# Kernel optimization log

Measured on AMD Instinct MI355X. Metric: run time of the kernel, lower is better.

The kernel has to match this reference:

```python
import jax, jax.numpy as jnp
import numpy as np

N_NODES = 50000
N_EDGES = 800000
IN_DIM = 256
HID = 64
NEG_SLOPE = 0.2


def setup_inputs() -> dict:
    key = jax.random.key(0)
    ks = jax.random.split(key, 16)
    s = lambda d: 1.0 / np.sqrt(d)
    x = jax.random.normal(ks[0], (N_NODES, IN_DIM), dtype=jnp.float32)
    src = jax.random.randint(ks[1], (N_EDGES,), 0, N_NODES, dtype=jnp.int32)
    dst = jax.random.randint(ks[2], (N_EDGES,), 0, N_NODES, dtype=jnp.int32)
    # layer 0: in 256 -> 4 heads x 64, no residual, ELU
    W0 = jax.random.normal(ks[3], (IN_DIM, 4 * HID), dtype=jnp.float32) * s(IN_DIM)
    al0 = jax.random.normal(ks[4], (4, HID), dtype=jnp.float32) * s(HID)
    ar0 = jax.random.normal(ks[5], (4, HID), dtype=jnp.float32) * s(HID)
    b0 = jnp.zeros((4 * HID,), dtype=jnp.float32)
    # layer 1: in 256 -> 4 heads x 64, identity residual (256 == 4*64), ELU
    W1 = jax.random.normal(ks[6], (4 * HID, 4 * HID), dtype=jnp.float32) * s(4 * HID)
    al1 = jax.random.normal(ks[7], (4, HID), dtype=jnp.float32) * s(HID)
    ar1 = jax.random.normal(ks[8], (4, HID), dtype=jnp.float32) * s(HID)
    b1 = jnp.zeros((4 * HID,), dtype=jnp.float32)
    # layer 2 (output): in 256 -> 1 head x 64, linear residual, no activation
    W2 = jax.random.normal(ks[9], (4 * HID, HID), dtype=jnp.float32) * s(4 * HID)
    al2 = jax.random.normal(ks[10], (1, HID), dtype=jnp.float32) * s(HID)
    ar2 = jax.random.normal(ks[11], (1, HID), dtype=jnp.float32) * s(HID)
    b2 = jnp.zeros((HID,), dtype=jnp.float32)
    res_w2 = jax.random.normal(ks[12], (4 * HID, HID), dtype=jnp.float32) * s(4 * HID)
    return {"x": x, "src": src, "dst": dst,
            "W0": W0, "al0": al0, "ar0": ar0, "b0": b0,
            "W1": W1, "al1": al1, "ar1": ar1, "b1": b1,
            "W2": W2, "al2": al2, "ar2": ar2, "b2": b2,
            "res_w2": res_w2}


def gat_layer(h, src, dst, W, al, ar, bias, residual, res_w, activation):
    H, D = al.shape
    feat = (h @ W).reshape(-1, H, D)               # [N,H,D]
    el = jnp.sum(feat * al[None], axis=-1)         # [N,H]
    er = jnp.sum(feat * ar[None], axis=-1)         # [N,H]
    e = jax.nn.leaky_relu(el[src] + er[dst], NEG_SLOPE)  # [E,H]
    # segment softmax over incoming edges of each destination node
    emax = jax.ops.segment_max(e, dst, num_segments=N_NODES)  # [N,H]
    ee = jnp.exp(e - emax[dst])
    denom = jax.ops.segment_sum(ee, dst, num_segments=N_NODES)
    alpha = ee / denom[dst]                        # [E,H]
    msg = feat[src] * alpha[..., None]             # [E,H,D]
    out = jax.ops.segment_sum(msg, dst, num_segments=N_NODES)  # [N,H,D]
    if residual:
        if res_w is not None:
            out = out + (h @ res_w).reshape(-1, 1, D)
        else:
            out = out + h.reshape(-1, H, D)
    out = out + bias.reshape(H, D)
    if activation:
        out = jax.nn.elu(out)
    return out.reshape(-1, H * D)                  # flatten(1)


def reference(x, src, dst, W0, al0, ar0, b0, W1, al1, ar1, b1,
              W2, al2, ar2, b2, res_w2):
    h = gat_layer(x, src, dst, W0, al0, ar0, b0, False, None, True)
    h = gat_layer(h, src, dst, W1, al1, ar1, b1, True, None, True)
    h = gat_layer(h, src, dst, W2, al2, ar2, b2, True, res_w2, False)
    return h  # [N, 64]
```

## Files before the change

kernel.cpp:

```cpp
#include <hip/hip_runtime.h>
#include <math.h>

#define NNODES 50000
#define NEDGES 800000

__device__ __forceinline__ float leaky(float x) { return x > 0.f ? x : 0.2f * x; }

__device__ __forceinline__ ushort f2bf(float f) {
    unsigned u = __float_as_uint(f);
    return (ushort)((u + 0x7fffu + ((u >> 16) & 1u)) >> 16);
}
__device__ __forceinline__ float bf2f(ushort u) {
    return __uint_as_float((unsigned)u << 16);
}

__global__ void hist_kernel(const int* __restrict__ dst, int* __restrict__ counts) {
    int e = blockIdx.x * 256 + threadIdx.x;
    if (e < NEDGES) atomicAdd(&counts[dst[e]], 1);
}

__global__ __launch_bounds__(256) void scan_partial(const int* __restrict__ counts,
                                                    int* __restrict__ bsum, int Nn) {
    int b = blockIdx.x, t = threadIdx.x;
    int base = b * 1024;
    int v = 0;
#pragma unroll
    for (int i = 0; i < 4; ++i) {
        int idx = base + t + 256 * i;
        if (idx < Nn) v += counts[idx];
    }
    for (int o = 32; o; o >>= 1) v += __shfl_xor(v, o);
    __shared__ int ws[4];
    if ((t & 63) == 0) ws[t >> 6] = v;
    __syncthreads();
    if (t == 0) bsum[b] = ws[0] + ws[1] + ws[2] + ws[3];
}

__global__ __launch_bounds__(256) void scan_final(const int* __restrict__ counts,
                                                  const int* __restrict__ bsum,
                                                  int* __restrict__ row_start, int Nn, int nB) {
    __shared__ int off_s;
    __shared__ int tsum[256];
    int b = blockIdx.x, t = threadIdx.x;
    if (t == 0) {
        int o = 0;
        for (int i = 0; i < b; ++i) o += bsum[i];
        off_s = o;
    }
    int base = b * 1024 + t * 4;
    int c0 = 0, c1 = 0, c2 = 0, c3 = 0;
    if (base + 3 < Nn) {
        int4 c = *reinterpret_cast<const int4*>(counts + base);
        c0 = c.x; c1 = c.y; c2 = c.z; c3 = c.w;
    } else {
        if (base + 0 < Nn) c0 = counts[base + 0];
        if (base + 1 < Nn) c1 = counts[base + 1];
        if (base + 2 < Nn) c2 = counts[base + 2];
        if (base + 3 < Nn) c3 = counts[base + 3];
    }
    int s0 = c0, s1 = s0 + c1, s2 = s1 + c2, s3 = s2 + c3;
    tsum[t] = s3;
    __syncthreads();
    for (int o = 1; o < 256; o <<= 1) {
        int u = (t >= o) ? tsum[t - o] : 0;
        __syncthreads();
        tsum[t] += u;
        __syncthreads();
    }
    int o = off_s + tsum[t] - s3;
    if (base + 3 < Nn) {
        *reinterpret_cast<int4*>(row_start + base) = make_int4(o, o + s0, o + s1, o + s2);
    } else {
        if (base + 0 < Nn) row_start[base + 0] = o;
        if (base + 1 < Nn) row_start[base + 1] = o + s0;
        if (base + 2 < Nn) row_start[base + 2] = o + s1;
        if (base + 3 < Nn) row_start[base + 3] = o + s2;
    }
    if (b == nB - 1 && t == 255) row_start[Nn] = off_s + tsum[255];
}

__global__ void scatter_kernel(const int* __restrict__ src, const int* __restrict__ dst,
                               const int* __restrict__ row_start, int* __restrict__ cursor,
                               int* __restrict__ csr_src) {
    int e = blockIdx.x * 256 + threadIdx.x;
    if (e < NEDGES) {
        int d = dst[e];
        int pos = row_start[d] + atomicAdd(&cursor[d], 1);
        csr_src[pos] = src[e];
    }
}

__global__ void pack_kernel(const float* __restrict__ W0, const float* __restrict__ W1,
                            const float* __restrict__ W2, const float* __restrict__ Wr,
                            ushort* __restrict__ Bt0, ushort* __restrict__ Bt1,
                            ushort* __restrict__ Bt2) {
    int idx = blockIdx.x * 256 + threadIdx.x;
    if (idx < 65536) {
        int n = idx >> 8, k = idx & 255;
        Bt0[idx] = f2bf(W0[k * 256 + n]);
    } else if (idx < 131072) {
        int j = idx - 65536;
        int n = j >> 8, k = j & 255;
        Bt1[j] = f2bf(W1[k * 256 + n]);
    } else {
        int j = idx - 131072;
        int n = j >> 8, k = j & 255;
        Bt2[j] = f2bf(n < 64 ? W2[k * 64 + n] : Wr[k * 64 + (n - 64)]);
    }
}

template <int MCOLS>
__global__ __launch_bounds__(256) void gemm_mfma(const float* __restrict__ A,
                                                 const ushort* __restrict__ Bt,
                                                 const float* __restrict__ al,
                                                 const float* __restrict__ ar,
                                                 ushort* __restrict__ featb,
                                                 float* __restrict__ el, float* __restrict__ er,
                                                 float* __restrict__ resid, int Nrows) {
    using bf16x8 = __attribute__((ext_vector_type(8))) short;
    using f32x4 = __attribute__((ext_vector_type(4))) float;
    __shared__ ushort As[8192];
    __shared__ ushort Bs[8192];
    const int tid = threadIdx.x;
    const int lane = tid & 63;
    const int wave = tid >> 6;
    const int wr = wave >> 1, wc = wave & 1;
    const int q = lane >> 4, li = lane & 15;
    const int r0 = blockIdx.x * 128;
    const int n0 = blockIdx.y * 128;

    f32x4 acc[4][4];
#pragma unroll
    for (int i = 0; i < 4; ++i)
#pragma unroll
        for (int j = 0; j < 4; ++j) acc[i][j] = (f32x4){0.f, 0.f, 0.f, 0.f};

    for (int kk = 0; kk < 256; kk += 64) {
        __syncthreads();
#pragma unroll
        for (int j = 0; j < 4; ++j) {
            int g = j * 256 + tid;
            int m = g >> 3, kg = g & 7;
            int mf = m >> 4, mr = m & 15;
            int row = r0 + m;
            float4 v0 = make_float4(0.f, 0.f, 0.f, 0.f), v1 = v0;
            if (row < Nrows) {
                const float* p = A + (size_t)row * 256 + kk + kg * 8;
                v0 = *reinterpret_cast<const float4*>(p);
                v1 = *reinterpret_cast<const float4*>(p + 4);
            }
            union { bf16x8 v; ushort u[8]; } pk;
            pk.u[0] = f2bf(v0.x); pk.u[1] = f2bf(v0.y);
            pk.u[2] = f2bf(v0.z); pk.u[3] = f2bf(v0.w);
            pk.u[4] = f2bf(v1.x); pk.u[5] = f2bf(v1.y);
            pk.u[6] = f2bf(v1.z); pk.u[7] = f2bf(v1.w);
            *reinterpret_cast<bf16x8*>(&As[((mf * 8 + kg) * 16 + (mr ^ kg)) * 8]) = pk.v;
        }
#pragma unroll
        for (int j = 0; j < 4; ++j) {
            int g = j * 256 + tid;
            int n = g >> 3, kg = g & 7;
            int nf = n >> 4, nr = n & 15;
            bf16x8 v = *reinterpret_cast<const bf16x8*>(Bt + (size_t)(n0 + n) * 256 + kk + kg * 8);
            *reinterpret_cast<bf16x8*>(&Bs[((nf * 8 + kg) * 16 + (nr ^ kg)) * 8]) = v;
        }
        __syncthreads();
#pragma unroll
        for (int t = 0; t < 2; ++t) {
            const int kc = t * 4 + q;
            bf16x8 af[4], bfv[4];
#pragma unroll
            for (int f = 0; f < 4; ++f) {
                af[f] = *reinterpret_cast<const bf16x8*>(
                    &As[(((wr * 4 + f) * 8 + kc) * 16 + (li ^ kc)) * 8]);
                bfv[f] = *reinterpret_cast<const bf16x8*>(
                    &Bs[(((wc * 4 + f) * 8 + kc) * 16 + (li ^ kc)) * 8]);
            }
#pragma unroll
            for (int f = 0; f < 4; ++f)
#pragma unroll
                for (int f2 = 0; f2 < 4; ++f2)
                    acc[f][f2] =
                        __builtin_amdgcn_mfma_f32_16x16x32_bf16(af[f], bfv[f2], acc[f][f2], 0, 0, 0);
        }
    }

    if constexpr (MCOLS == 256) {
        const int hblk = (n0 >> 6) + wc;
        float alv[4], arv[4];
#pragma unroll
        for (int f2 = 0; f2 < 4; ++f2) {
            alv[f2] = al[hblk * 64 + f2 * 16 + li];
            arv[f2] = ar[hblk * 64 + f2 * 16 + li];
        }
#pragma unroll
        for (int f = 0; f < 4; ++f) {
#pragma unroll
            for (int r = 0; r < 4; ++r) {
                int row = r0 + wr * 64 + f * 16 + q * 4 + r;
                bool ok = row < Nrows;
                float elp = 0.f, erp = 0.f;
#pragma unroll
                for (int f2 = 0; f2 < 4; ++f2) {
                    float v = acc[f][f2][r];
                    elp = fmaf(v, alv[f2], elp);
                    erp = fmaf(v, arv[f2], erp);
                    if (ok) featb[(size_t)row * 256 + (f2 * 16 + li) * 4 + hblk] = f2bf(v);
                }
#pragma unroll
                for (int o = 1; o < 16; o <<= 1) {
                    elp += __shfl_xor(elp, o);
                    erp += __shfl_xor(erp, o);
                }
                if (ok && li == 0) {
                    el[row * 4 + hblk] = elp;
                    er[row * 4 + hblk] = erp;
                }
            }
        }
    } else {
        if (wc == 0) {
            float alv[4], arv[4];
#pragma unroll
            for (int f2 = 0; f2 < 4; ++f2) {
                alv[f2] = al[f2 * 16 + li];
                arv[f2] = ar[f2 * 16 + li];
            }
#pragma unroll
            for (int f = 0; f < 4; ++f) {
#pragma unroll
                for (int r = 0; r < 4; ++r) {
                    int row = r0 + wr * 64 + f * 16 + q * 4 + r;
                    bool ok = row < Nrows;
                    float elp = 0.f, erp = 0.f;
#pragma unroll
                    for (int f2 = 0; f2 < 4; ++f2) {
                        float v = acc[f][f2][r];
                        elp = fmaf(v, alv[f2], elp);
                        erp = fmaf(v, arv[f2], erp);
                        if (ok) featb[(size_t)row * 64 + f2 * 16 + li] = f2bf(v);
                    }
#pragma unroll
                    for (int o = 1; o < 16; o <<= 1) {
                        elp += __shfl_xor(elp, o);
                        erp += __shfl_xor(erp, o);
                    }
                    if (ok && li == 0) {
                        el[row] = elp;
                        er[row] = erp;
                    }
                }
            }
        } else {
#pragma unroll
            for (int f = 0; f < 4; ++f) {
#pragma unroll
                for (int r = 0; r < 4; ++r) {
                    int row = r0 + wr * 64 + f * 16 + q * 4 + r;
                    if (row < Nrows) {
#pragma unroll
                        for (int f2 = 0; f2 < 4; ++f2)
                            resid[(size_t)row * 64 + f2 * 16 + li] = acc[f][f2][r];
                    }
                }
            }
        }
    }
}

template <int RES, bool ACT>
__global__ __launch_bounds__(256) void agg4_kernel(
    const ushort* __restrict__ featb, const float* __restrict__ el,
    const float* __restrict__ er, const int* __restrict__ row_start,
    const int* __restrict__ csr_src, const float* __restrict__ resbuf,
    const float* __restrict__ bias, float* __restrict__ out, int Nn) {
    using ushort8v = __attribute__((ext_vector_type(8))) unsigned short;
    __shared__ float wbuf[4][256];
    __shared__ int obuf[4][64];
    const int wv = threadIdx.x >> 6, lane = threadIdx.x & 63;
    const int g = lane >> 5, li = lane & 31;
    int node = blockIdx.x * 4 + wv;
    if (node >= Nn) return;

    int begin = row_start[node], end = row_start[node + 1];
    float4 ern = *(reinterpret_cast<const float4*>(er) + node);

    float denom[4] = {0.f, 0.f, 0.f, 0.f};
    float acc[2][4] = {{0.f, 0.f, 0.f, 0.f}, {0.f, 0.f, 0.f, 0.f}};

    for (int c = begin; c < end; c += 64) {
        int nE = min(64, end - c);
        float4 w = make_float4(0.f, 0.f, 0.f, 0.f);
        int s = 0;
        if (lane < nE) {
            s = csr_src[c + lane];
            float4 e4 = *(reinterpret_cast<const float4*>(el) + s);
            w.x = __expf(leaky(e4.x + ern.x));
            w.y = __expf(leaky(e4.y + ern.y));
            w.z = __expf(leaky(e4.z + ern.z));
            w.w = __expf(leaky(e4.w + ern.w));
        }
        denom[0] += w.x; denom[1] += w.y; denom[2] += w.z; denom[3] += w.w;
        obuf[wv][lane] = s * 256;
        *reinterpret_cast<float4*>(&wbuf[wv][lane * 4]) = w;
        __asm__ volatile("s_waitcnt lgkmcnt(0)" ::: "memory");

#pragma unroll 4
        for (int e2 = 0; e2 < nE; e2 += 2) {
            int e = e2 + g;
            float4 we = make_float4(0.f, 0.f, 0.f, 0.f);
            int off = 0;
            if (e < nE) {
                off = obuf[wv][e];
                we = *reinterpret_cast<const float4*>(&wbuf[wv][e * 4]);
            }
            ushort8v v = *reinterpret_cast<const ushort8v*>(featb + off + li * 8);
            acc[0][0] = fmaf(we.x, bf2f(v[0]), acc[0][0]);
            acc[0][1] = fmaf(we.y, bf2f(v[1]), acc[0][1]);
            acc[0][2] = fmaf(we.z, bf2f(v[2]), acc[0][2]);
            acc[0][3] = fmaf(we.w, bf2f(v[3]), acc[0][3]);
            acc[1][0] = fmaf(we.x, bf2f(v[4]), acc[1][0]);
            acc[1][1] = fmaf(we.y, bf2f(v[5]), acc[1][1]);
            acc[1][2] = fmaf(we.z, bf2f(v[6]), acc[1][2]);
            acc[1][3] = fmaf(we.w, bf2f(v[7]), acc[1][3]);
        }
        __asm__ volatile("" ::: "memory");
    }

#pragma unroll
    for (int j = 0; j < 2; ++j)
#pragma unroll
        for (int h = 0; h < 4; ++h) acc[j][h] += __shfl_xor(acc[j][h], 32);
#pragma unroll
    for (int h = 0; h < 4; ++h)
        for (int o = 32; o; o >>= 1) denom[h] += __shfl_xor(denom[h], o);

    bool has = end > begin;
#pragma unroll
    for (int hh = 0; hh < 2; ++hh) {
        int h = g * 2 + hh;
        float d0 = denom[h];
        float o0 = has ? acc[0][h] / d0 : 0.f;
        float o1 = has ? acc[1][h] / d0 : 0.f;
        int dbase = h * 64 + li * 2;
        if constexpr (RES == 1) {
            float2 rv = *reinterpret_cast<const float2*>(resbuf + (size_t)node * 256 + dbase);
            o0 += rv.x; o1 += rv.y;
        }
        float2 bv = *reinterpret_cast<const float2*>(bias + dbase);
        o0 += bv.x; o1 += bv.y;
        if constexpr (ACT) {
            o0 = o0 > 0.f ? o0 : __expf(o0) - 1.f;
            o1 = o1 > 0.f ? o1 : __expf(o1) - 1.f;
        }
        *reinterpret_cast<float2*>(out + (size_t)node * 256 + dbase) = make_float2(o0, o1);
    }
}

__global__ __launch_bounds__(256) void agg1_kernel(
    const ushort* __restrict__ featb, const float* __restrict__ el,
    const float* __restrict__ er, const int* __restrict__ row_start,
    const int* __restrict__ csr_src, const float* __restrict__ resbuf,
    const float* __restrict__ bias, float* __restrict__ out, int Nn) {
    __shared__ float wbuf[4][64];
    __shared__ int obuf[4][64];
    const int wv = threadIdx.x >> 6, lane = threadIdx.x & 63;
    const int g = lane >> 4, li = lane & 15;
    int node = blockIdx.x * 4 + wv;
    if (node >= Nn) return;

    int begin = row_start[node], end = row_start[node + 1];
    float ern = er[node];
    float denom = 0.f;
    float acc[4] = {0.f, 0.f, 0.f, 0.f};

    for (int c = begin; c < end; c += 64) {
        int nE = min(64, end - c);
        float w = 0.f;
        int s = 0;
        if (lane < nE) {
            s = csr_src[c + lane];
            w = __expf(leaky(el[s] + ern));
        }
        denom += w;
        obuf[wv][lane] = s * 64;
        wbuf[wv][lane] = w;
        __asm__ volatile("s_waitcnt lgkmcnt(0)" ::: "memory");

#pragma unroll 2
        for (int e4i = 0; e4i < nE; e4i += 4) {
            int e = e4i + g;
            float we = 0.f;
            int off = 0;
            if (e < nE) {
                off = obuf[wv][e];
                we = wbuf[wv][e];
            }
            ushort4 v = *reinterpret_cast<const ushort4*>(featb + off + li * 4);
            acc[0] = fmaf(we, bf2f(v.x), acc[0]);
            acc[1] = fmaf(we, bf2f(v.y), acc[1]);
            acc[2] = fmaf(we, bf2f(v.z), acc[2]);
            acc[3] = fmaf(we, bf2f(v.w), acc[3]);
        }
        __asm__ volatile("" ::: "memory");
    }

#pragma unroll
    for (int j = 0; j < 4; ++j) {
        acc[j] += __shfl_xor(acc[j], 16);
        acc[j] += __shfl_xor(acc[j], 32);
    }
    for (int o = 32; o; o >>= 1) denom += __shfl_xor(denom, o);

    if (g == 0) {
        bool has = end > begin;
        float4 rv = *reinterpret_cast<const float4*>(resbuf + (size_t)node * 64 + li * 4);
        float4 bv = *reinterpret_cast<const float4*>(bias + li * 4);
        float4 o4;
        o4.x = (has ? acc[0] / denom : 0.f) + rv.x + bv.x;
        o4.y = (has ? acc[1] / denom : 0.f) + rv.y + bv.y;
        o4.z = (has ? acc[2] / denom : 0.f) + rv.z + bv.z;
        o4.w = (has ? acc[3] / denom : 0.f) + rv.w + bv.w;
        *reinterpret_cast<float4*>(out + (size_t)node * 64 + li * 4) = o4;
    }
}

extern "C" void kernel_launch(void* const* d_in, const int* in_sizes, int n_in, void* d_out,
                              int out_size, void* d_ws, size_t ws_size, hipStream_t stream) {
    const float* x   = (const float*)d_in[0];
    const int* src   = (const int*)d_in[1];
    const int* dst   = (const int*)d_in[2];
    const float* W0  = (const float*)d_in[3];
    const float* al0 = (const float*)d_in[4];
    const float* ar0 = (const float*)d_in[5];
    const float* b0  = (const float*)d_in[6];
    const float* W1  = (const float*)d_in[7];
    const float* al1 = (const float*)d_in[8];
    const float* ar1 = (const float*)d_in[9];
    const float* b1  = (const float*)d_in[10];
    const float* W2  = (const float*)d_in[11];
    const float* al2 = (const float*)d_in[12];
    const float* ar2 = (const float*)d_in[13];
    const float* b2  = (const float*)d_in[14];
    const float* Wr2 = (const float*)d_in[15];
    float* out = (float*)d_out;

    char* w = (char*)d_ws;
    size_t off = 0;
    auto alloc = [&](size_t bytes) -> char* {
        char* p = w + off;
        off += (bytes + 255) & ~(size_t)255;
        return p;
    };
    float* hbuf     = (float*)alloc((size_t)NNODES * 256 * 4);
    ushort* featb   = (ushort*)alloc((size_t)NNODES * 256 * 2);
    float* resid    = (float*)alloc((size_t)NNODES * 64 * 4);
    float* el       = (float*)alloc((size_t)NNODES * 4 * 4);
    float* er       = (float*)alloc((size_t)NNODES * 4 * 4);
    ushort* Bt0     = (ushort*)alloc(65536 * 2);
    ushort* Bt1     = (ushort*)alloc(65536 * 2);
    ushort* Bt2     = (ushort*)alloc(32768 * 2);
    int* counts     = (int*)alloc((size_t)NNODES * 4 * 2);
    int* cursor     = counts + NNODES;
    int* row_start  = (int*)alloc((size_t)(NNODES + 1) * 4);
    int* bsum       = (int*)alloc(64 * 4);
    int* csr_src    = (int*)alloc((size_t)NEDGES * 4);

    hipMemsetAsync(counts, 0, (size_t)NNODES * 4 * 2, stream);

    const int EB = (NEDGES + 255) / 256;
    const int NB4 = (NNODES + 3) / 4;
    const int NBM = (NNODES + 127) / 128;
    const int NSB = (NNODES + 1023) / 1024;

    hist_kernel<<<EB, 256, 0, stream>>>(dst, counts);
    scan_partial<<<NSB, 256, 0, stream>>>(counts, bsum, NNODES);
    scan_final<<<NSB, 256, 0, stream>>>(counts, bsum, row_start, NNODES, NSB);
    scatter_kernel<<<EB, 256, 0, stream>>>(src, dst, row_start, cursor, csr_src);
    pack_kernel<<<640, 256, 0, stream>>>(W0, W1, W2, Wr2, Bt0, Bt1, Bt2);

    gemm_mfma<256><<<dim3(NBM, 2), 256, 0, stream>>>(x, Bt0, al0, ar0, featb, el, er,
                                                     nullptr, NNODES);
    agg4_kernel<0, true><<<NB4, 256, 0, stream>>>(featb, el, er, row_start, csr_src,
                                                  nullptr, b0, hbuf, NNODES);
    gemm_mfma<256><<<dim3(NBM, 2), 256, 0, stream>>>(hbuf, Bt1, al1, ar1, featb, el, er,
                                                     nullptr, NNODES);
    agg4_kernel<1, true><<<NB4, 256, 0, stream>>>(featb, el, er, row_start, csr_src,
                                                  hbuf, b1, hbuf, NNODES);
    gemm_mfma<128><<<dim3(NBM, 1), 256, 0, stream>>>(hbuf, Bt2, al2, ar2, featb, el, er,
                                                     resid, NNODES);
    agg1_kernel<<<NB4, 256, 0, stream>>>(featb, el, er, row_start, csr_src,
                                         resid, b2, out, NNODES);
}
```

Baseline: 457.3 us.

## Store hidden activations in bf16 and load GEMM tiles directly into LDS

Hidden-layer activations between layers are now stored as bf16 instead of fp32, halving the buffer traffic for aggregation writes, residual reads and GEMM A-loads. The later GEMMs then stage A and B tiles with global_load_lds straight into shared memory, using an unswizzled layout, which removes the in-register conversion and copy. The scan-partial and weight-pack kernels are merged into one launch. In exchange, the residual path loses precision through bf16 rounding, and the unswizzled LDS layout may cause bank conflicts.

```diff
diff --git a/kernel.cpp b/kernel.cpp
--- a/kernel.cpp
+++ b/kernel.cpp
@@ -3,6 +3,7 @@
 
 #define NNODES 50000
 #define NEDGES 800000
+#define NSB 49
 
 __device__ __forceinline__ float leaky(float x) { return x > 0.f ? x : 0.2f * x; }
 
@@ -14,26 +15,49 @@
     return __uint_as_float((unsigned)u << 16);
 }
 
+typedef const __attribute__((address_space(1))) void* gptr_t;
+typedef __attribute__((address_space(3))) void* lptr_t;
+
 __global__ void hist_kernel(const int* __restrict__ dst, int* __restrict__ counts) {
     int e = blockIdx.x * 256 + threadIdx.x;
     if (e < NEDGES) atomicAdd(&counts[dst[e]], 1);
 }
 
-__global__ __launch_bounds__(256) void scan_partial(const int* __restrict__ counts,
-                                                    int* __restrict__ bsum, int Nn) {
-    int b = blockIdx.x, t = threadIdx.x;
-    int base = b * 1024;
-    int v = 0;
-#pragma unroll
-    for (int i = 0; i < 4; ++i) {
-        int idx = base + t + 256 * i;
-        if (idx < Nn) v += counts[idx];
-    }
-    for (int o = 32; o; o >>= 1) v += __shfl_xor(v, o);
-    __shared__ int ws[4];
-    if ((t & 63) == 0) ws[t >> 6] = v;
-    __syncthreads();
-    if (t == 0) bsum[b] = ws[0] + ws[1] + ws[2] + ws[3];
+__global__ __launch_bounds__(256) void prep_kernel(
+    const int* __restrict__ counts, int* __restrict__ bsum, int Nn,
+    const float* __restrict__ W0, const float* __restrict__ W1, const float* __restrict__ W2,
+    const float* __restrict__ Wr, ushort* __restrict__ Bt0, ushort* __restrict__ Bt1,
+    ushort* __restrict__ Bt2) {
+    int t = threadIdx.x;
+    if (blockIdx.x < NSB) {
+        int b = blockIdx.x;
+        int base = b * 1024;
+        int v = 0;
+#pragma unroll
+        for (int i = 0; i < 4; ++i) {
+            int idx = base + t + 256 * i;
+            if (idx < Nn) v += counts[idx];
+        }
+        for (int o = 32; o; o >>= 1) v += __shfl_xor(v, o);
+        __shared__ int ws[4];
+        if ((t & 63) == 0) ws[t >> 6] = v;
+        __syncthreads();
+        if (t == 0) bsum[b] = ws[0] + ws[1] + ws[2] + ws[3];
+    } else {
+        int idx = (blockIdx.x - NSB) * 256 + t;
+        if (idx < 65536) {
+            int n = idx >> 8, k = idx & 255;
+            Bt0[idx] = f2bf(W0[k * 256 + n]);
+        } else if (idx < 131072) {
+            int j = idx - 65536;
+            int n = j >> 8, k = j & 255;
+            Bt1[j] = f2bf(W1[k * 256 + n]);
+        } else {
+            int j = idx - 131072;
+            int n = j >> 8, k = j & 255;
+            Bt2[j] = f2bf(n < 64 ? W2[k * 64 + n] : Wr[k * 64 + (n - 64)]);
+        }
+    }
 }
 
 __global__ __launch_bounds__(256) void scan_final(const int* __restrict__ counts,
@@ -90,27 +114,8 @@
     }
 }
 
-__global__ void pack_kernel(const float* __restrict__ W0, const float* __restrict__ W1,
-                            const float* __restrict__ W2, const float* __restrict__ Wr,
-                            ushort* __restrict__ Bt0, ushort* __restrict__ Bt1,
-                            ushort* __restrict__ Bt2) {
-    int idx = blockIdx.x * 256 + threadIdx.x;
-    if (idx < 65536) {
-        int n = idx >> 8, k = idx & 255;
-        Bt0[idx] = f2bf(W0[k * 256 + n]);
-    } else if (idx < 131072) {
-        int j = idx - 65536;
-        int n = j >> 8, k = j & 255;
-        Bt1[j] = f2bf(W1[k * 256 + n]);
-    } else {
-        int j = idx - 131072;
-        int n = j >> 8, k = j & 255;
-        Bt2[j] = f2bf(n < 64 ? W2[k * 64 + n] : Wr[k * 64 + (n - 64)]);
-    }
-}
-
-template <int MCOLS>
-__global__ __launch_bounds__(256) void gemm_mfma(const float* __restrict__ A,
+template <int MCOLS, bool ABF16>
+__global__ __launch_bounds__(256) void gemm_mfma(const void* __restrict__ Araw,
                                                  const ushort* __restrict__ Bt,
                                                  const float* __restrict__ al,
                                                  const float* __restrict__ ar,
@@ -121,6 +126,8 @@
     using f32x4 = __attribute__((ext_vector_type(4))) float;
     __shared__ ushort As[8192];
     __shared__ ushort Bs[8192];
+    const float* Af = (const float*)Araw;
+    const ushort* Ab = (const ushort*)Araw;
     const int tid = threadIdx.x;
     const int lane = tid & 63;
     const int wave = tid >> 6;
@@ -137,32 +144,43 @@
 
     for (int kk = 0; kk < 256; kk += 64) {
         __syncthreads();
+        if constexpr (ABF16) {
+#pragma unroll
+            for (int j = 0; j < 4; ++j) {
+                int c = (wave * 4 + j) * 64 + lane;
+                int mr = c & 15, kg = (c >> 4) & 7, mf = c >> 7;
+                const ushort* gp = Ab + (size_t)(r0 + mf * 16 + mr) * 256 + kk + kg * 8;
+                void* lp = (char*)As + (size_t)(wave * 4 + j) * 1024;
+                __builtin_amdgcn_global_load_lds((gptr_t)gp, (lptr_t)lp, 16, 0, 0);
+            }
+        } else {
+#pragma unroll
+            for (int j = 0; j < 4; ++j) {
+                int g = j * 256 + tid;
+                int m = g >> 3, kg = g & 7;
+                int mf = m >> 4, mr = m & 15;
+                int row = r0 + m;
+                float4 v0 = make_float4(0.f, 0.f, 0.f, 0.f), v1 = v0;
+                if (row < Nrows) {
+                    const float* p = Af + (size_t)row * 256 + kk + kg * 8;
+                    v0 = *reinterpret_cast<const float4*>(p);
+                    v1 = *reinterpret_cast<const float4*>(p + 4);
+                }
+                union { bf16x8 v; ushort u[8]; } pk;
+                pk.u[0] = f2bf(v0.x); pk.u[1] = f2bf(v0.y);
+                pk.u[2] = f2bf(v0.z); pk.u[3] = f2bf(v0.w);
+                pk.u[4] = f2bf(v1.x); pk.u[5] = f2bf(v1.y);
+                pk.u[6] = f2bf(v1.z); pk.u[7] = f2bf(v1.w);
+                *reinterpret_cast<bf16x8*>(&As[((mf * 8 + kg) * 16 + (mr ^ kg)) * 8]) = pk.v;
+            }
+        }
 #pragma unroll
         for (int j = 0; j < 4; ++j) {
-            int g = j * 256 + tid;
-            int m = g >> 3, kg = g & 7;
-            int mf = m >> 4, mr = m & 15;
-            int row = r0 + m;
-            float4 v0 = make_float4(0.f, 0.f, 0.f, 0.f), v1 = v0;
-            if (row < Nrows) {
-                const float* p = A + (size_t)row * 256 + kk + kg * 8;
-                v0 = *reinterpret_cast<const float4*>(p);
-                v1 = *reinterpret_cast<const float4*>(p + 4);
-            }
-            union { bf16x8 v; ushort u[8]; } pk;
-            pk.u[0] = f2bf(v0.x); pk.u[1] = f2bf(v0.y);
-            pk.u[2] = f2bf(v0.z); pk.u[3] = f2bf(v0.w);
-            pk.u[4] = f2bf(v1.x); pk.u[5] = f2bf(v1.y);
-            pk.u[6] = f2bf(v1.z); pk.u[7] = f2bf(v1.w);
-            *reinterpret_cast<bf16x8*>(&As[((mf * 8 + kg) * 16 + (mr ^ kg)) * 8]) = pk.v;
-        }
-#pragma unroll
-        for (int j = 0; j < 4; ++j) {
-            int g = j * 256 + tid;
-            int n = g >> 3, kg = g & 7;
-            int nf = n >> 4, nr = n & 15;
-            bf16x8 v = *reinterpret_cast<const bf16x8*>(Bt + (size_t)(n0 + n) * 256 + kk + kg * 8);
-            *reinterpret_cast<bf16x8*>(&Bs[((nf * 8 + kg) * 16 + (nr ^ kg)) * 8]) = v;
+            int c = (wave * 4 + j) * 64 + lane;
+            int nr = c & 15, kg = (c >> 4) & 7, nf = c >> 7;
+            const ushort* gp = Bt + (size_t)(n0 + nf * 16 + nr) * 256 + kk + kg * 8;
+            void* lp = (char*)Bs + (size_t)(wave * 4 + j) * 1024;
+            __builtin_amdgcn_global_load_lds((gptr_t)gp, (lptr_t)lp, 16, 0, 0);
         }
         __syncthreads();
 #pragma unroll
@@ -171,10 +189,11 @@
             bf16x8 af[4], bfv[4];
 #pragma unroll
             for (int f = 0; f < 4; ++f) {
+                int ai = ABF16 ? li : (li ^ kc);
                 af[f] = *reinterpret_cast<const bf16x8*>(
-                    &As[(((wr * 4 + f) * 8 + kc) * 16 + (li ^ kc)) * 8]);
+                    &As[(((wr * 4 + f) * 8 + kc) * 16 + ai) * 8]);
                 bfv[f] = *reinterpret_cast<const bf16x8*>(
-                    &Bs[(((wc * 4 + f) * 8 + kc) * 16 + (li ^ kc)) * 8]);
+                    &Bs[(((wc * 4 + f) * 8 + kc) * 16 + li) * 8]);
             }
 #pragma unroll
             for (int f = 0; f < 4; ++f)
@@ -272,8 +291,8 @@
 __global__ __launch_bounds__(256) void agg4_kernel(
     const ushort* __restrict__ featb, const float* __restrict__ el,
     const float* __restrict__ er, const int* __restrict__ row_start,
-    const int* __restrict__ csr_src, const float* __restrict__ resbuf,
-    const float* __restrict__ bias, float* __restrict__ out, int Nn) {
+    const int* __restrict__ csr_src, const ushort* __restrict__ resbuf,
+    const float* __restrict__ bias, ushort* __restrict__ out, int Nn) {
     using ushort8v = __attribute__((ext_vector_type(8))) unsigned short;
     __shared__ float wbuf[4][256];
     __shared__ int obuf[4][64];
@@ -344,8 +363,9 @@
         float o1 = has ? acc[1][h] / d0 : 0.f;
         int dbase = h * 64 + li * 2;
         if constexpr (RES == 1) {
-            float2 rv = *reinterpret_cast<const float2*>(resbuf + (size_t)node * 256 + dbase);
-            o0 += rv.x; o1 += rv.y;
+            unsigned rv = *reinterpret_cast<const unsigned*>(resbuf + (size_t)node * 256 + dbase);
+            o0 += bf2f((ushort)(rv & 0xffffu));
+            o1 += bf2f((ushort)(rv >> 16));
         }
         float2 bv = *reinterpret_cast<const float2*>(bias + dbase);
         o0 += bv.x; o1 += bv.y;
@@ -353,7 +373,8 @@
             o0 = o0 > 0.f ? o0 : __expf(o0) - 1.f;
             o1 = o1 > 0.f ? o1 : __expf(o1) - 1.f;
         }
-        *reinterpret_cast<float2*>(out + (size_t)node * 256 + dbase) = make_float2(o0, o1);
+        unsigned pk = (unsigned)f2bf(o0) | ((unsigned)f2bf(o1) << 16);
+        *reinterpret_cast<unsigned*>(out + (size_t)node * 256 + dbase) = pk;
     }
 }
 
@@ -452,7 +473,7 @@
         off += (bytes + 255) & ~(size_t)255;
         return p;
     };
-    float* hbuf     = (float*)alloc((size_t)NNODES * 256 * 4);
+    ushort* hbuf    = (ushort*)alloc((size_t)NNODES * 256 * 2);
     ushort* featb   = (ushort*)alloc((size_t)NNODES * 256 * 2);
     float* resid    = (float*)alloc((size_t)NNODES * 64 * 4);
     float* el       = (float*)alloc((size_t)NNODES * 4 * 4);
@@ -471,24 +492,23 @@
     const int EB = (NEDGES + 255) / 256;
     const int NB4 = (NNODES + 3) / 4;
     const int NBM = (NNODES + 127) / 128;
-    const int NSB = (NNODES + 1023) / 1024;
 
     hist_kernel<<<EB, 256, 0, stream>>>(dst, counts);
-    scan_partial<<<NSB, 256, 0, stream>>>(counts, bsum, NNODES);
+    prep_kernel<<<NSB + 640, 256, 0, stream>>>(counts, bsum, NNODES, W0, W1, W2, Wr2,
+                                               Bt0, Bt1, Bt2);
     scan_final<<<NSB, 256, 0, stream>>>(counts, bsum, row_start, NNODES, NSB);
     scatter_kernel<<<EB, 256, 0, stream>>>(src, dst, row_start, cursor, csr_src);
-    pack_kernel<<<640, 256, 0, stream>>>(W0, W1, W2, Wr2, Bt0, Bt1, Bt2);
-
-    gemm_mfma<256><<<dim3(NBM, 2), 256, 0, stream>>>(x, Bt0, al0, ar0, featb, el, er,
-                                                     nullptr, NNODES);
+
+    gemm_mfma<256, false><<<dim3(NBM, 2), 256, 0, stream>>>(x, Bt0, al0, ar0, featb, el, er,
+                                                            nullptr, NNODES);
     agg4_kernel<0, true><<<NB4, 256, 0, stream>>>(featb, el, er, row_start, csr_src,
                                                   nullptr, b0, hbuf, NNODES);
-    gemm_mfma<256><<<dim3(NBM, 2), 256, 0, stream>>>(hbuf, Bt1, al1, ar1, featb, el, er,
-                                                     nullptr, NNODES);
+    gemm_mfma<256, true><<<dim3(NBM, 2), 256, 0, stream>>>(hbuf, Bt1, al1, ar1, featb, el, er,
+                                                           nullptr, NNODES);
     agg4_kernel<1, true><<<NB4, 256, 0, stream>>>(featb, el, er, row_start, csr_src,
                                                   hbuf, b1, hbuf, NNODES);
-    gemm_mfma<128><<<dim3(NBM, 1), 256, 0, stream>>>(hbuf, Bt2, al2, ar2, featb, el, er,
-                                                     resid, NNODES);
+    gemm_mfma<128, true><<<dim3(NBM, 1), 256, 0, stream>>>(hbuf, Bt2, al2, ar2, featb, el, er,
+                                                           resid, NNODES);
     agg1_kernel<<<NB4, 256, 0, stream>>>(featb, el, er, row_start, csr_src,
                                          resid, b2, out, NNODES);
 }
```

Measured after the change: 446.9 us. 2.3% less time.
